# Kernel tuning notes

Measured on AMD Instinct MI355X. Metric: run time of the kernel, lower is better.

The kernel has to match this reference:

```python
import jax, jax.numpy as jnp
import numpy as np

EMB, GCN = 256, 256
N_REL = 200
B, E, TOPK = 256, 100000, 64
N_PREV, N_ENT, N_TIME = 50000, 20000, 2000


def _linear(x, w, b):
    # torch nn.Linear convention: w is [out, in]
    return x @ w.T + b


def setup_inputs() -> dict:
    key = jax.random.key(0)
    ks = jax.random.split(key, 32)
    nrm = lambda k, s: (jax.random.normal(k, s, jnp.float32) * 0.05)
    # facts columns: b, n, h, r, t, ts. b built so every batch has >= TOPK facts.
    b_col = jax.random.permutation(ks[0], jnp.arange(E, dtype=jnp.int32) % B)
    n_col = jax.random.randint(ks[1], (E,), 0, N_PREV, jnp.int32)
    h_col = jax.random.randint(ks[2], (E,), 0, N_ENT, jnp.int32)
    r_col = jax.random.randint(ks[3], (E,), 0, N_REL, jnp.int32)  # r+1 indexes [zero;rel]
    t_col = jax.random.randint(ks[4], (E,), 0, N_ENT, jnp.int32)
    ts_col = jax.random.randint(ks[5], (E,), 0, N_TIME, jnp.int32)
    facts = jnp.stack([b_col, n_col, h_col, r_col, t_col, ts_col], axis=1)
    return {
        "query_time": jax.random.randint(ks[6], (B,), 0, N_TIME, jnp.int32),  # unused by forward
        "query_emd": nrm(ks[7], (B, EMB)),
        "temp_neighbors_facts": facts,
        "ent_emd": nrm(ks[8], (N_ENT, GCN)),
        "rel_emd": nrm(ks[9], (N_REL, GCN)),
        "hidden_node": nrm(ks[10], (N_PREV, EMB)),
        "hidden_rel": nrm(ks[11], (N_PREV, EMB)),
        "hidden_time": nrm(ks[12], (N_PREV, EMB)),  # unused by forward
        "att_agg": jax.random.uniform(ks[13], (N_PREV,), jnp.float32),
        "time_emd": nrm(ks[14], (N_TIME, EMB)),
        "zero_rel_emd": nrm(ks[15], (1, GCN)),
        "W_message_w": nrm(ks[16], (EMB, 2 * EMB)), "W_message_b": jnp.zeros((EMB,), jnp.float32),
        "att_1_w": nrm(ks[17], (1, 3 * EMB)), "att_1_b": jnp.zeros((1,), jnp.float32),
        "att_2_w": nrm(ks[18], (1, EMB)), "att_2_b": jnp.zeros((1,), jnp.float32),
        "W_h_w": nrm(ks[19], (EMB, 2 * EMB)), "W_h_b": jnp.zeros((EMB,), jnp.float32),
        "lin_e_ts_w": nrm(ks[20], (EMB, GCN + EMB)), "lin_e_ts_b": jnp.zeros((EMB,), jnp.float32),
        "lin_r_ts_w": nrm(ks[21], (EMB, GCN)), "lin_r_ts_b": jnp.zeros((EMB,), jnp.float32),
        "lin_time_w": nrm(ks[22], (EMB, EMB)), "lin_time_b": jnp.zeros((EMB,), jnp.float32),
        "gru_w_ih": nrm(ks[23], (3 * EMB, EMB)), "gru_w_hh": nrm(ks[24], (3 * EMB, EMB)),
        "gru_b_ih": jnp.zeros((3 * EMB,), jnp.float32), "gru_b_hh": jnp.zeros((3 * EMB,), jnp.float32),
        "batch_size": B, "device": 0, "max_nodes": TOPK,
    }


def reference(query_time, query_emd, temp_neighbors_facts, ent_emd, rel_emd,
              hidden_node, hidden_rel, hidden_time, att_agg, time_emd,
              zero_rel_emd, W_message_w, W_message_b, att_1_w, att_1_b,
              att_2_w, att_2_b, W_h_w, W_h_b, lin_e_ts_w, lin_e_ts_b,
              lin_r_ts_w, lin_r_ts_b, lin_time_w, lin_time_b,
              gru_w_ih, gru_w_hh, gru_b_ih, gru_b_hh,
              batch_size, device, max_nodes):
    f = temp_neighbors_facts
    b, n, r, t, ts = f[:, 0], f[:, 1], f[:, 3], f[:, 4], f[:, 5]

    hidden_node_pre = hidden_node[n]            # [E, EMB]
    hidden_rel_pre = hidden_rel[n]              # [E, EMB]
    rel_all = jnp.concatenate([zero_rel_emd, rel_emd], axis=0)
    h_r = rel_all[r + 1]                        # [E, GCN]
    h_ts_raw = time_emd[ts]                     # [E, EMB]
    h_t = _linear(jnp.concatenate([ent_emd[t], h_ts_raw], -1), lin_e_ts_w, lin_e_ts_b)
    h_r = _linear(h_r, lin_r_ts_w, lin_r_ts_b)
    _ = _linear(h_ts_raw, lin_time_w, lin_time_b)  # computed but unused in original

    message = _linear(jnp.concatenate([hidden_node_pre, h_r], -1), W_message_w, W_message_b)
    att_input = jnp.concatenate([query_emd[b], message, h_t], -1)  # [E, 3*EMB]
    att1 = jax.nn.sigmoid(_linear(att_input, att_1_w, att_1_b))[:, 0]

    # single-step GRU (torch nn.GRU gate math)
    gi = h_r @ gru_w_ih.T + gru_b_ih            # [E, 3*EMB]
    gh = hidden_rel_pre @ gru_w_hh.T + gru_b_hh
    i_r, i_z, i_n = jnp.split(gi, 3, axis=-1)
    h_rg, h_zg, h_ng = jnp.split(gh, 3, axis=-1)
    rg = jax.nn.sigmoid(i_r + h_rg)
    zg = jax.nn.sigmoid(i_z + h_zg)
    ng = jnp.tanh(i_n + rg * h_ng)
    hidden_rel_new = (1.0 - zg) * ng + zg * hidden_rel_pre

    att2 = jax.nn.sigmoid(_linear(hidden_rel_new, att_2_w, att_2_b))[:, 0]
    attention = (att1 + att2) * 0.5

    # vectorized per-batch top-k (each batch is guaranteed >= max_nodes facts)
    order = jnp.lexsort((-attention, b))        # sort by batch asc, attention desc
    counts = jax.ops.segment_sum(jnp.ones_like(b), b, num_segments=batch_size)
    starts = jnp.cumsum(counts) - counts
    sel = (starts[:, None] + jnp.arange(max_nodes)[None, :]).reshape(-1)
    new_index = order[sel]                      # [B*topk]

    facts_k = f[new_index]
    message = message[new_index]
    hidden_rel_new = hidden_rel_new[new_index]
    attention = (att1[new_index] + att2[new_index]) * 0.5
    b_k, n_k = facts_k[:, 0], facts_k[:, 1]
    attention = attention * att_agg[n_k]
    M = b_k.shape[0]

    rows = facts_k[:, jnp.array([0, 4, 5])]     # (b, t, ts)
    tail_nodes, tail_index = jnp.unique(rows, axis=0, size=M, fill_value=0, return_inverse=True)
    tail_index = tail_index.reshape(-1)

    tail_emd = _linear(jnp.concatenate([ent_emd[tail_nodes[:, 1]], time_emd[tail_nodes[:, 2]]], -1),
                       lin_e_ts_w, lin_e_ts_b)

    # group_max_norm: normalize attention by per-batch sum (0/0 -> 0)
    den = jax.ops.segment_sum(attention, b_k, num_segments=batch_size)[b_k]
    safe_den = jnp.where(den != 0, den, 1.0)
    attention = jnp.where(den != 0, attention / safe_den, 0.0)

    message_agg = jax.ops.segment_sum(attention[:, None] * message, tail_index, num_segments=M)
    hidden_node_new = _linear(jnp.concatenate([message_agg, tail_emd], -1), W_h_w, W_h_b)  # act = identity
    hidden_rel_out = jax.ops.segment_sum(attention[:, None] * hidden_rel_new, tail_index, num_segments=M)
    att_agg_new = jax.ops.segment_sum(attention, tail_index, num_segments=M)
    return tail_nodes, hidden_node_new, hidden_rel_out, att_agg_new
```

## Files before the change

kernel.cpp:

```cpp
#include <hip/hip_runtime.h>
#include <hip/hip_bf16.h>

#define E_N    100000
#define B_N    256
#define TOPK   64
#define NPREV  50000
#define NENT   20000
#define NTIME  2000
#define NREL   200
#define M_OUT  16384
#define NTILE  3125

static __device__ __forceinline__ float sigm(float x){ return 1.f/(1.f+expf(-x)); }

__global__ void zero_kernel(unsigned* __restrict__ p, int n){
  int i = blockIdx.x*256 + threadIdx.x;
  if (i < n) p[i] = 0u;
}

__global__ void pack_w_kernel(const float* __restrict__ w_msg,
                              const float* __restrict__ w_hh,
                              float4* __restrict__ wP){
  int i = blockIdx.x*256 + threadIdx.x;
  if (i < 65536){
    int t = i & 255;
    int mat = (i >> 8) & 3;
    int kblk = i >> 10;
    float4 v;
    if (mat == 0) v = *(const float4*)&w_msg[(size_t)t*512 + kblk*4];
    else          v = *(const float4*)&w_hh[(size_t)((mat-1)*256 + t)*256 + kblk*4];
    wP[i] = v;
  }
}

__global__ void matvec_fused(const float* __restrict__ w_msg,
                             const float* __restrict__ lets_w,
                             const float* __restrict__ lets_b,
                             const float* __restrict__ att1w,
                             const float* __restrict__ att1b,
                             float* __restrict__ wm1a, float* __restrict__ ve,
                             float* __restrict__ vts, float* __restrict__ consts){
  int blk = blockIdx.x, t = threadIdx.x;
  if (blk == 3){
    if (t < 64){
      float p = 0.f;
      for (int d = t; d < 256; d += 64) p += lets_b[d]*att1w[512+d];
      for (int o = 32; o > 0; o >>= 1) p += __shfl_down(p, o);
      if (t == 0) consts[0] = att1b[0] + p;
    }
    return;
  }
  const float* M; int moff; const float* v; float* out;
  if (blk == 0){ M = w_msg;  moff = 0;   v = att1w+256; out = wm1a; }
  else if (blk == 1){ M = lets_w; moff = 0;   v = att1w+512; out = ve; }
  else { M = lets_w; moff = 256; v = att1w+512; out = vts; }
  float acc = 0.f;
  for (int d = 0; d < 256; ++d) acc += M[(size_t)d*512 + moff + t] * v[d];
  out[t] = acc;
}

__global__ void rows_dot_multi(
    const float* __restrict__ A0, const float* __restrict__ v0, float* __restrict__ o0, int n0,
    const float* __restrict__ A1, const float* __restrict__ v1, float* __restrict__ o1_, int n1,
    const float* __restrict__ A2, const float* __restrict__ v2, float* __restrict__ o2, int n2,
    const float* __restrict__ A3, const float* __restrict__ v3, float* __restrict__ o3, int n3,
    const float* __restrict__ A4, const float* __restrict__ v4, float* __restrict__ o4, int n4){
  int gid = blockIdx.x*256 + threadIdx.x;
  int wid = gid >> 6, lane = gid & 63;
  const float* A; const float* v; float* o; int r;
  if (wid < n0){ A=A0; v=v0; o=o0; r=wid; }
  else if ((wid -= n0) < n1){ A=A1; v=v1; o=o1_; r=wid; }
  else if ((wid -= n1) < n2){ A=A2; v=v2; o=o2; r=wid; }
  else if ((wid -= n2) < n3){ A=A3; v=v3; o=o3; r=wid; }
  else if ((wid -= n3) < n4){ A=A4; v=v4; o=o4; r=wid; }
  else return;
  const float* row = A + (size_t)r*256;
  float p = 0.f;
  for (int k = lane; k < 256; k += 64) p += row[k]*v[k];
  for (int off = 32; off > 0; off >>= 1) p += __shfl_down(p, off);
  if (lane == 0) o[r] = p;
}

template<int ND>
__global__ __launch_bounds__(256) void tile_linear(
    const float* __restrict__ A, int lda,
    const float* __restrict__ Bw, int ldb, int boff,
    const float* __restrict__ bias,
    float* __restrict__ out, int ldo, int rows){
  __shared__ float a_s[16][260];
  int tile0 = blockIdx.x*16;
  for (int idx = threadIdx.x; idx < 16*256; idx += 256){
    int i = idx >> 8, k = idx & 255;
    int row = tile0 + i;
    a_s[i][k] = (row < rows) ? A[(size_t)row*lda + k] : 0.f;
  }
  __syncthreads();
  int d = threadIdx.x;
  const float* brow[ND];
  #pragma unroll
  for (int q = 0; q < ND; ++q) brow[q] = Bw + (size_t)(d + 256*q)*ldb + boff;
  float acc[ND][16];
  #pragma unroll
  for (int q = 0; q < ND; ++q){
    float bv = bias ? bias[d + 256*q] : 0.f;
    #pragma unroll
    for (int i = 0; i < 16; ++i) acc[q][i] = bv;
  }
  for (int k = 0; k < 256; k += 4){
    float4 w[ND];
    #pragma unroll
    for (int q = 0; q < ND; ++q) w[q] = *(const float4*)(brow[q] + k);
    #pragma unroll
    for (int i = 0; i < 16; ++i){
      float4 a = *(const float4*)&a_s[i][k];
      #pragma unroll
      for (int q = 0; q < ND; ++q)
        acc[q][i] += w[q].x*a.x + w[q].y*a.y + w[q].z*a.z + w[q].w*a.w;
    }
  }
  #pragma unroll
  for (int i = 0; i < 16; ++i){
    int row = tile0 + i;
    if (row < rows){
      #pragma unroll
      for (int q = 0; q < ND; ++q) out[(size_t)row*ldo + d + 256*q] = acc[q][i];
    }
  }
}

__global__ void hist_kernel(const int* __restrict__ facts, int* __restrict__ cnt){
  int e = blockIdx.x*256 + threadIdx.x;
  if (e < E_N) atomicAdd(&cnt[facts[e*6+1] >> 4], 1);
}

__global__ void bin_scan_kernel(const int* __restrict__ cnt, int* __restrict__ off,
                                int* __restrict__ cur){
  int lane = threadIdx.x;
  int run = 0;
  for (int base = 0; base < 3136; base += 64){
    int idx = base + lane;
    int orig = (idx < NTILE) ? cnt[idx] : 0;
    int v = orig;
    for (int o = 1; o < 64; o <<= 1){ int t = __shfl_up(v, o); if (lane >= o) v += t; }
    if (idx < NTILE){ int ex = run + v - orig; off[idx] = ex; cur[idx] = ex; }
    run += __shfl(v, 63);
  }
  if (lane == 0) off[NTILE] = E_N;
}

__global__ void scatter_kernel(const int* __restrict__ facts, int* __restrict__ cur,
                               int* __restrict__ edges){
  int e = blockIdx.x*256 + threadIdx.x;
  if (e < E_N){
    int p = atomicAdd(&cur[facts[e*6+1] >> 4], 1);
    edges[p] = e;
  }
}

__global__ __launch_bounds__(256) void att_kernel(
    const float* __restrict__ hidden_rel,
    const float4* __restrict__ wP,
    const float* __restrict__ b_hh,
    const float* __restrict__ gi,
    const float* __restrict__ att2w, const float* __restrict__ att2b,
    const int* __restrict__ facts,
    const int* __restrict__ bin_off, const int* __restrict__ bin_edges,
    const float* __restrict__ qdot, const float* __restrict__ sn_m,
    const float* __restrict__ sr_m, const float* __restrict__ se,
    const float* __restrict__ st,   const float* __restrict__ consts,
    float* __restrict__ attention){
  __shared__ float gh_s[16][776];
  int tile0 = blockIdx.x*16;
  int t = threadIdx.x;

  float acc[3][16];
  #pragma unroll
  for (int q = 0; q < 3; ++q)
    #pragma unroll
    for (int p = 0; p < 16; ++p) acc[q][p] = 0.f;

  float4 w1 = wP[256 + t], w2 = wP[512 + t], w3 = wP[768 + t];
  for (int kb = 0; kb < 64; ++kb){
    int kbn = (kb + 1) & 63;
    int nb = (kbn*4)*256 + t;
    float4 nw1 = wP[nb + 256], nw2 = wP[nb + 512], nw3 = wP[nb + 768];
    int k = kb*4;
    #pragma unroll
    for (int p = 0; p < 16; ++p){
      float4 a = *(const float4*)&hidden_rel[(size_t)(tile0+p)*256 + k];
      acc[0][p] += w1.x*a.x + w1.y*a.y + w1.z*a.z + w1.w*a.w;
      acc[1][p] += w2.x*a.x + w2.y*a.y + w2.z*a.z + w2.w*a.w;
      acc[2][p] += w3.x*a.x + w3.y*a.y + w3.z*a.z + w3.w*a.w;
    }
    w1 = nw1; w2 = nw2; w3 = nw3;
  }
  #pragma unroll
  for (int q = 0; q < 3; ++q){
    float bv = b_hh[t + 256*q];
    #pragma unroll
    for (int p = 0; p < 16; ++p)
      gh_s[p][t + 256*q] = acc[q][p] + bv;
  }
  __syncthreads();

  int wv = t >> 6, l = t & 63;
  int o0 = bin_off[blockIdx.x], o1 = bin_off[blockIdx.x + 1];
  int d0 = 4*l;
  float4 a2 = *(const float4*)&att2w[d0];
  float c1 = consts[0];
  float a2b = att2b[0];
  for (int idx = o0 + wv; idx < o1; idx += 4){
    int e  = bin_edges[idx];
    int b  = facts[e*6+0], n = facts[e*6+1], r = facts[e*6+3];
    int t_ = facts[e*6+4], ts_ = facts[e*6+5];
    int nl = n - tile0;
    float4 ghr = *(const float4*)&gh_s[nl][d0];
    float4 ghz = *(const float4*)&gh_s[nl][256+d0];
    float4 ghn = *(const float4*)&gh_s[nl][512+d0];
    const float* girow = gi + (size_t)r*768;
    float4 gir = *(const float4*)&girow[d0];
    float4 giz = *(const float4*)&girow[256+d0];
    float4 gin = *(const float4*)&girow[512+d0];
    float4 hp  = *(const float4*)&hidden_rel[(size_t)n*256 + d0];
    float partial;
    {
      float rg = sigm(gir.x + ghr.x), zg = sigm(giz.x + ghz.x);
      float ng = tanhf(gin.x + rg*ghn.x);
      partial = a2.x * ((1.f - zg)*ng + zg*hp.x);
    }{
      float rg = sigm(gir.y + ghr.y), zg = sigm(giz.y + ghz.y);
      float ng = tanhf(gin.y + rg*ghn.y);
      partial += a2.y * ((1.f - zg)*ng + zg*hp.y);
    }{
      float rg = sigm(gir.z + ghr.z), zg = sigm(giz.z + ghz.z);
      float ng = tanhf(gin.z + rg*ghn.z);
      partial += a2.z * ((1.f - zg)*ng + zg*hp.z);
    }{
      float rg = sigm(gir.w + ghr.w), zg = sigm(giz.w + ghz.w);
      float ng = tanhf(gin.w + rg*ghn.w);
      partial += a2.w * ((1.f - zg)*ng + zg*hp.w);
    }
    #pragma unroll
    for (int o = 32; o > 0; o >>= 1) partial += __shfl_xor(partial, o);
    if (l == 0){
      float att2 = sigm(partial + a2b);
      float x1 = qdot[b] + sn_m[n] + sr_m[r] + se[t_] + st[ts_] + c1;
      attention[e] = 0.5f*(sigm(x1) + att2);
    }
  }
}

__global__ __launch_bounds__(256) void topk_kernel(
    const int* __restrict__ facts, const float* __restrict__ attention,
    const float* __restrict__ att_agg,
    int* __restrict__ sel_edge, float* __restrict__ att_norm,
    unsigned* __restrict__ skey, int* __restrict__ Ub){
  __shared__ float sa[512];
  __shared__ int   si[512];
  __shared__ unsigned sk[64];
  __shared__ int cnt;
  int b = blockIdx.x, tid = threadIdx.x;
  sa[tid] = -1.f; sa[tid+256] = -1.f;
  si[tid] = 0x7fffffff; si[tid+256] = 0x7fffffff;
  if (tid == 0) cnt = 0;
  __syncthreads();
  for (int e = tid; e < E_N; e += 256){
    if (facts[e*6] == b){
      int p = atomicAdd(&cnt, 1);
      if (p < 512){ sa[p] = attention[e]; si[p] = e; }
    }
  }
  __syncthreads();
  for (int k = 2; k <= 512; k <<= 1){
    for (int j = k >> 1; j > 0; j >>= 1){
      for (int i0 = tid; i0 < 512; i0 += 256){
        int l = i0 ^ j;
        if (l > i0){
          float ai = sa[i0], al = sa[l];
          int   ii = si[i0], il = si[l];
          bool lFirst = (al > ai) || (al == ai && il < ii);
          bool up = ((i0 & k) == 0);
          if (up ? lFirst : !lFirst){
            sa[i0] = al; sa[l] = ai; si[i0] = il; si[l] = ii;
          }
        }
      }
      __syncthreads();
    }
  }
  if (tid < 64){
    int e = si[tid];
    bool valid = (e != 0x7fffffff);
    if (!valid) e = 0;
    int n = facts[e*6+1];
    float a = valid ? sa[tid]*att_agg[n] : 0.f;
    float den = a;
    for (int o = 32; o > 0; o >>= 1) den += __shfl_down(den, o);
    den = __shfl(den, 0);
    float norm = (den != 0.f) ? a/den : 0.f;
    sel_edge[b*64 + tid] = e;
    att_norm[b*64 + tid] = norm;
    int t_ = facts[e*6+4], ts_ = facts[e*6+5];
    unsigned key = (((unsigned)t_) << 11) | (unsigned)ts_;
    sk[tid] = (key << 6) | (unsigned)tid;
  }
  __syncthreads();
  for (int k = 2; k <= 64; k <<= 1){
    for (int j = k >> 1; j > 0; j >>= 1){
      unsigned nv = 0; bool act = tid < 64;
      if (act){
        unsigned mine = sk[tid], other = sk[tid ^ j];
        bool up = ((tid & k) == 0);
        bool keepmin = (up == ((tid & j) == 0));
        nv = keepmin ? (mine < other ? mine : other) : (mine > other ? mine : other);
      }
      __syncthreads();
      if (act) sk[tid] = nv;
      __syncthreads();
    }
  }
  if (tid < 64){
    unsigned kk = sk[tid];
    skey[b*64 + tid] = kk;
    bool head = (tid == 0) || ((kk >> 6) != (sk[tid-1] >> 6));
    unsigned long long bal = __ballot(head);
    if (tid == 0) Ub[b] = __popcll(bal);
  }
}

__global__ void offs_scan_kernel(const int* __restrict__ Ub, int* __restrict__ offs){
  int lane = threadIdx.x;
  int run = 0;
  for (int base = 0; base < 256; base += 64){
    int orig = Ub[base + lane];
    int v = orig;
    for (int o = 1; o < 64; o <<= 1){ int t = __shfl_up(v, o); if (lane >= o) v += t; }
    offs[base + lane] = run + v - orig;
    run += __shfl(v, 63);
  }
  if (lane == 0) offs[256] = run;
}

__global__ void emit_kernel(const unsigned* __restrict__ skey, const int* __restrict__ offs,
                            int* __restrict__ us, int* __restrict__ tails,
                            float* __restrict__ out_tail){
  int b = blockIdx.x, tid = threadIdx.x;
  unsigned kk = skey[b*64 + tid];
  bool head = (tid == 0) || ((kk >> 6) != (skey[b*64 + tid - 1] >> 6));
  unsigned long long bal = __ballot(head);
  unsigned long long mask_le = (tid == 63) ? ~0ull : ((1ull << (tid+1)) - 1ull);
  int ulocal = __popcll(bal & mask_le) - 1;
  int u = offs[b] + ulocal;
  us[b*64 + tid] = u;
  if (head){
    unsigned key = kk >> 6;
    int t_ = (int)(key >> 11), ts_ = (int)(key & 2047u);
    tails[u*3+0] = b; tails[u*3+1] = t_; tails[u*3+2] = ts_;
    out_tail[u*3+0] = (float)b;
    out_tail[u*3+1] = (float)t_;
    out_tail[u*3+2] = (float)ts_;
  }
}

__global__ __launch_bounds__(256) void sel_kernel(
    const unsigned* __restrict__ skey, const int* __restrict__ sel_edge,
    const float* __restrict__ att_norm, const int* __restrict__ facts,
    const float* __restrict__ hidden_node, const float* __restrict__ hidden_rel,
    const float4* __restrict__ wP,
    const float* __restrict__ msg_r, const float* __restrict__ gi,
    const float* __restrict__ b_hh,
    float* __restrict__ msg_sel, float* __restrict__ hrn_sel){
  __shared__ int n_s[8], r_s[8];
  __shared__ float av_s[8];
  int base = blockIdx.x*8;
  int t = threadIdx.x;
  if (t < 8){
    int gs = base + t;
    int b = gs >> 6, i = gs & 63;
    int j = (int)(skey[(size_t)b*64 + i] & 63u);
    int s = b*64 + j;
    int e = sel_edge[s];
    n_s[t] = facts[e*6+1];
    r_s[t] = facts[e*6+3];
    av_s[t] = att_norm[s];
  }
  __syncthreads();

  float acc[4][8];
  #pragma unroll
  for (int q = 0; q < 4; ++q)
    #pragma unroll
    for (int e = 0; e < 8; ++e) acc[q][e] = 0.f;

  float4 w0 = wP[t], w1 = wP[256 + t], w2 = wP[512 + t], w3 = wP[768 + t];
  for (int kb = 0; kb < 64; ++kb){
    int kbn = (kb + 1) & 63;
    int nb = (kbn*4)*256 + t;
    float4 nw0 = wP[nb], nw1 = wP[nb + 256], nw2 = wP[nb + 512], nw3 = wP[nb + 768];
    int k = kb*4;
    #pragma unroll
    for (int e = 0; e < 8; ++e){
      float4 an = *(const float4*)&hidden_node[(size_t)n_s[e]*256 + k];
      float4 ah = *(const float4*)&hidden_rel[(size_t)n_s[e]*256 + k];
      acc[0][e] += w0.x*an.x + w0.y*an.y + w0.z*an.z + w0.w*an.w;
      acc[1][e] += w1.x*ah.x + w1.y*ah.y + w1.z*ah.z + w1.w*ah.w;
      acc[2][e] += w2.x*ah.x + w2.y*ah.y + w2.z*ah.z + w2.w*ah.w;
      acc[3][e] += w3.x*ah.x + w3.y*ah.y + w3.z*ah.z + w3.w*ah.w;
    }
    w0 = nw0; w1 = nw1; w2 = nw2; w3 = nw3;
  }

  float bhr = b_hh[t], bhz = b_hh[256+t], bhn = b_hh[512+t];
  #pragma unroll
  for (int e = 0; e < 8; ++e){
    int r = r_s[e]; float a = av_s[e];
    const float* girow = gi + (size_t)r*768;
    float msgv = acc[0][e] + msg_r[(size_t)r*256 + t];
    float rg = sigm(girow[t]      + acc[1][e] + bhr);
    float zg = sigm(girow[256+t]  + acc[2][e] + bhz);
    float ng = tanhf(girow[512+t] + rg*(acc[3][e] + bhn));
    float hp = hidden_rel[(size_t)n_s[e]*256 + t];
    float hrn = (1.f - zg)*ng + zg*hp;
    size_t o = (size_t)(base + e)*256 + t;
    msg_sel[o] = a*msgv;
    hrn_sel[o] = a*hrn;
  }
}

__global__ __launch_bounds__(256) void segsum_kernel(
    const unsigned* __restrict__ skey, const int* __restrict__ us,
    const float* __restrict__ att_norm,
    const float* __restrict__ msg_sel, const float* __restrict__ hrn_sel,
    float* __restrict__ msg_agg, float* __restrict__ out_hrel,
    float* __restrict__ out_aagg){
  int b = blockIdx.x, d = threadIdx.x;
  float accm = 0.f, acch = 0.f, acca = 0.f;
  int ucur = -1;
  for (int i = 0; i < 64; ++i){
    int u = us[b*64 + i];
    if (u != ucur){
      if (ucur >= 0){
        msg_agg[(size_t)ucur*256 + d] = accm;
        out_hrel[(size_t)ucur*256 + d] = acch;
        if (d == 0) out_aagg[ucur] = acca;
      }
      ucur = u; accm = 0.f; acch = 0.f; acca = 0.f;
    }
    size_t o = (size_t)(b*64 + i)*256 + d;
    accm += msg_sel[o];
    acch += hrn_sel[o];
    int j = (int)(skey[b*64 + i] & 63u);
    acca += att_norm[b*64 + j];
  }
  if (ucur >= 0){
    msg_agg[(size_t)ucur*256 + d] = accm;
    out_hrel[(size_t)ucur*256 + d] = acch;
    if (d == 0) out_aagg[ucur] = acca;
  }
}

__global__ __launch_bounds__(256) void final_kernel(
    const float* __restrict__ msg_agg, const int* __restrict__ tails,
    const float* __restrict__ ent_t, const float* __restrict__ time_t,
    const float* __restrict__ w_h, const float* __restrict__ b_h,
    float* __restrict__ out_hn){
  __shared__ float x_s[16][520];
  int tile0 = blockIdx.x*16;
  for (int idx = threadIdx.x; idx < 16*512; idx += 256){
    int i = idx >> 9, k = idx & 511;
    int u = tile0 + i;
    float v;
    if (k < 256) v = msg_agg[(size_t)u*256 + k];
    else {
      int kk = k - 256;
      v = ent_t[(size_t)tails[u*3+1]*256 + kk] + time_t[(size_t)tails[u*3+2]*256 + kk];
    }
    x_s[i][k] = v;
  }
  __syncthreads();
  int d = threadIdx.x;
  const float* wrow = w_h + (size_t)d*512;
  float bv = b_h[d];
  float acc[16];
  #pragma unroll
  for (int i = 0; i < 16; ++i) acc[i] = bv;
  for (int k = 0; k < 512; k += 4){
    float4 w = *(const float4*)(wrow + k);
    #pragma unroll
    for (int i = 0; i < 16; ++i){
      float4 a = *(const float4*)&x_s[i][k];
      acc[i] += w.x*a.x + w.y*a.y + w.z*a.z + w.w*a.w;
    }
  }
  #pragma unroll
  for (int i = 0; i < 16; ++i)
    out_hn[(size_t)(tile0+i)*256 + d] = acc[i];
}

extern "C" void kernel_launch(void* const* d_in, const int* in_sizes, int n_in,
                              void* d_out, int out_size, void* d_ws, size_t ws_size,
                              hipStream_t stream){
  const float* query_emd   = (const float*)d_in[1];
  const int*   facts       = (const int*)  d_in[2];
  const float* ent_emd     = (const float*)d_in[3];
  const float* rel_emd     = (const float*)d_in[4];
  const float* hidden_node = (const float*)d_in[5];
  const float* hidden_rel  = (const float*)d_in[6];
  const float* att_agg     = (const float*)d_in[8];
  const float* time_emd    = (const float*)d_in[9];
  const float* w_msg       = (const float*)d_in[11];
  const float* b_msg       = (const float*)d_in[12];
  const float* att1w       = (const float*)d_in[13];
  const float* att1b       = (const float*)d_in[14];
  const float* att2w       = (const float*)d_in[15];
  const float* att2b       = (const float*)d_in[16];
  const float* w_h         = (const float*)d_in[17];
  const float* b_h         = (const float*)d_in[18];
  const float* lets_w      = (const float*)d_in[19];
  const float* lets_b      = (const float*)d_in[20];
  const float* lrts_w      = (const float*)d_in[21];
  const float* lrts_b      = (const float*)d_in[22];
  const float* w_ih        = (const float*)d_in[25];
  const float* w_hh        = (const float*)d_in[26];
  const float* b_ih        = (const float*)d_in[27];
  const float* b_hh        = (const float*)d_in[28];

  char* p = (char*)d_ws;
  auto alloc = [&](size_t bytes) -> void* {
    void* r = (void*)p; p += (bytes + 255) & ~(size_t)255; return r;
  };
  int* bin_cnt  = (int*)alloc(3136*4);
  int* bin_cur  = (int*)alloc(3136*4);
  int* tails    = (int*)alloc((size_t)M_OUT*3*4);
  float* msg_agg= (float*)alloc((size_t)M_OUT*256*4);
  size_t zero_words = (3136*4 + 3136*4 + (size_t)M_OUT*3*4 + (size_t)M_OUT*256*4) / 4;
  int* bin_off  = (int*)alloc(3136*4);
  int* bin_edges= (int*)alloc(E_N*4);
  float* attention = (float*)alloc(E_N*4);
  float* qdot   = (float*)alloc(256*4);
  float* sn_m   = (float*)alloc(NPREV*4);
  float* se     = (float*)alloc(NENT*4);
  float* st     = (float*)alloc(NTIME*4);
  float* sr_m   = (float*)alloc(NREL*4);
  float* wm1a   = (float*)alloc(256*4);
  float* ve     = (float*)alloc(256*4);
  float* vts    = (float*)alloc(256*4);
  float* consts = (float*)alloc(8*4);
  float* hr2    = (float*)alloc((size_t)NREL*256*4);
  float* msg_r  = (float*)alloc((size_t)NREL*256*4);
  float* gi     = (float*)alloc((size_t)NREL*768*4);
  float* time_t = (float*)alloc((size_t)NTIME*256*4);
  float* ent_t  = (float*)alloc((size_t)NENT*256*4);
  float4* wP    = (float4*)alloc((size_t)65536*16);
  int* sel_edge = (int*)alloc(M_OUT*4);
  float* att_nrm= (float*)alloc(M_OUT*4);
  unsigned* skey= (unsigned*)alloc(M_OUT*4);
  int* Ub       = (int*)alloc(256*4);
  int* offs     = (int*)alloc(257*4);
  int* us       = (int*)alloc(M_OUT*4);
  float* msg_sel= (float*)alloc((size_t)M_OUT*256*4);
  float* hrn_sel= (float*)alloc((size_t)M_OUT*256*4);
  (void)ws_size; (void)in_sizes; (void)n_in;

  float* out_f     = (float*)d_out;
  float* out_tail  = out_f;
  float* out_hn    = out_f + (size_t)M_OUT*3;
  float* out_hrel  = out_f + (size_t)M_OUT*3 + (size_t)M_OUT*256;
  float* out_aagg  = out_f + (size_t)M_OUT*3 + (size_t)2*M_OUT*256;

  zero_kernel<<<(out_size+255)/256, 256, 0, stream>>>((unsigned*)d_out, out_size);
  zero_kernel<<<((int)zero_words+255)/256, 256, 0, stream>>>((unsigned*)bin_cnt, (int)zero_words);

  pack_w_kernel<<<256, 256, 0, stream>>>(w_msg, w_hh, wP);
  matvec_fused<<<4, 256, 0, stream>>>(w_msg, lets_w, lets_b, att1w, att1b, wm1a, ve, vts, consts);

  tile_linear<1><<<(NREL+15)/16, 256, 0, stream>>>(rel_emd, 256, lrts_w, 256, 0, lrts_b, hr2, 256, NREL);
  tile_linear<1><<<(NREL+15)/16, 256, 0, stream>>>(hr2, 256, w_msg, 512, 256, b_msg, msg_r, 256, NREL);
  tile_linear<3><<<(NREL+15)/16, 256, 0, stream>>>(hr2, 256, w_ih, 256, 0, b_ih, gi, 768, NREL);
  tile_linear<1><<<(NTIME+15)/16, 256, 0, stream>>>(time_emd, 256, lets_w, 512, 256, (const float*)nullptr, time_t, 256, NTIME);
  tile_linear<1><<<(NENT+15)/16, 256, 0, stream>>>(ent_emd, 256, lets_w, 512, 0, lets_b, ent_t, 256, NENT);

  {
    int total_rows = B_N + NPREV + NENT + NTIME + NREL;
    int blocks = (total_rows*64 + 255)/256;
    rows_dot_multi<<<blocks, 256, 0, stream>>>(
        query_emd, att1w, qdot, B_N,
        hidden_node, wm1a, sn_m, NPREV,
        ent_emd, ve, se, NENT,
        time_emd, vts, st, NTIME,
        msg_r, att1w+256, sr_m, NREL);
  }

  hist_kernel<<<(E_N+255)/256, 256, 0, stream>>>(facts, bin_cnt);
  bin_scan_kernel<<<1, 64, 0, stream>>>(bin_cnt, bin_off, bin_cur);
  scatter_kernel<<<(E_N+255)/256, 256, 0, stream>>>(facts, bin_cur, bin_edges);

  att_kernel<<<NTILE, 256, 0, stream>>>(hidden_rel, wP, b_hh, gi, att2w, att2b,
      facts, bin_off, bin_edges, qdot, sn_m, sr_m, se, st, consts, attention);

  topk_kernel<<<B_N, 256, 0, stream>>>(facts, attention, att_agg, sel_edge, att_nrm, skey, Ub);
  offs_scan_kernel<<<1, 64, 0, stream>>>(Ub, offs);
  emit_kernel<<<B_N, 64, 0, stream>>>(skey, offs, us, tails, out_tail);
  sel_kernel<<<M_OUT/8, 256, 0, stream>>>(skey, sel_edge, att_nrm, facts,
      hidden_node, hidden_rel, wP, msg_r, gi, b_hh, msg_sel, hrn_sel);
  segsum_kernel<<<B_N, 256, 0, stream>>>(skey, us, att_nrm, msg_sel, hrn_sel,
      msg_agg, out_hrel, out_aagg);
  final_kernel<<<M_OUT/16, 256, 0, stream>>>(msg_agg, tails, ent_t, time_t, w_h, b_h, out_hn);
}
```

Before: 1.190 ms.

## Bucket facts per batch for topk, halve att tiles, use packed weights in GEMVs

The per-batch topk gather used to scan all 100k facts in every block. It now reads a CSR of edges per batch, built during the same histogram, scan and scatter passes as the node-tile binning. Node tiles in the attention kernel shrink from 16 to 8 rows, which doubles the block count and lowers register use. The ent/time projections and the final W_h linear now read k-blocked float4 weight layouts packed up front, and the final kernel no longer stages through shared memory. The costs are more atomics in scatter, extra packing work, and a hidden_rel GEMV whose weight traffic is amortised over fewer rows.

```diff
diff --git a/kernel.cpp b/kernel.cpp
--- a/kernel.cpp
+++ b/kernel.cpp
@@ -9,7 +9,7 @@
 #define NTIME  2000
 #define NREL   200
 #define M_OUT  16384
-#define NTILE  3125
+#define NT8    6250
 
 static __device__ __forceinline__ float sigm(float x){ return 1.f/(1.f+expf(-x)); }
 
@@ -20,16 +20,26 @@
 
 __global__ void pack_w_kernel(const float* __restrict__ w_msg,
                               const float* __restrict__ w_hh,
-                              float4* __restrict__ wP){
+                              const float* __restrict__ lets_w,
+                              const float* __restrict__ w_h,
+                              float4* __restrict__ wP,
+                              float4* __restrict__ wPL,
+                              float4* __restrict__ wPH){
   int i = blockIdx.x*256 + threadIdx.x;
   if (i < 65536){
-    int t = i & 255;
-    int mat = (i >> 8) & 3;
-    int kblk = i >> 10;
+    int t = i & 255, mat = (i >> 8) & 3, kblk = i >> 10;
     float4 v;
     if (mat == 0) v = *(const float4*)&w_msg[(size_t)t*512 + kblk*4];
     else          v = *(const float4*)&w_hh[(size_t)((mat-1)*256 + t)*256 + kblk*4];
     wP[i] = v;
+  } else if (i < 98304){
+    int j = i - 65536;
+    int t = j & 255, mat = (j >> 8) & 1, kblk = j >> 9;
+    wPL[j] = *(const float4*)&lets_w[(size_t)t*512 + mat*256 + kblk*4];
+  } else if (i < 131072){
+    int j = i - 98304;
+    int t = j & 255, kblk = j >> 8;
+    wPH[j] = *(const float4*)&w_h[(size_t)t*512 + kblk*4];
   }
 }
 
@@ -128,32 +138,68 @@
   }
 }
 
-__global__ void hist_kernel(const int* __restrict__ facts, int* __restrict__ cnt){
+__global__ __launch_bounds__(256) void gemv_ets(
+    const float* __restrict__ act, const float4* __restrict__ wPL, int matsel,
+    const float* __restrict__ bias, float* __restrict__ out){
+  int tile0 = blockIdx.x*16, t = threadIdx.x;
+  float acc[16];
+  float bv = bias ? bias[t] : 0.f;
+  #pragma unroll
+  for (int p = 0; p < 16; ++p) acc[p] = bv;
+  float4 w = wPL[matsel*256 + t];
+  for (int kb = 0; kb < 64; ++kb){
+    int kbn = (kb + 1) & 63;
+    float4 nw = wPL[(kbn*2 + matsel)*256 + t];
+    int k = kb*4;
+    #pragma unroll
+    for (int p = 0; p < 16; ++p){
+      float4 a = *(const float4*)&act[(size_t)(tile0+p)*256 + k];
+      acc[p] += w.x*a.x + w.y*a.y + w.z*a.z + w.w*a.w;
+    }
+    w = nw;
+  }
+  #pragma unroll
+  for (int p = 0; p < 16; ++p)
+    out[(size_t)(tile0+p)*256 + t] = acc[p];
+}
+
+__global__ void hist2_kernel(const int* __restrict__ facts,
+                             int* __restrict__ cnt_t, int* __restrict__ cnt_b){
   int e = blockIdx.x*256 + threadIdx.x;
-  if (e < E_N) atomicAdd(&cnt[facts[e*6+1] >> 4], 1);
-}
-
-__global__ void bin_scan_kernel(const int* __restrict__ cnt, int* __restrict__ off,
-                                int* __restrict__ cur){
+  if (e < E_N){
+    atomicAdd(&cnt_t[facts[e*6+1] >> 3], 1);
+    atomicAdd(&cnt_b[facts[e*6+0]], 1);
+  }
+}
+
+__global__ void scan2_kernel(const int* __restrict__ cnt_t, int* __restrict__ off_t, int* __restrict__ cur_t,
+                             const int* __restrict__ cnt_b, int* __restrict__ off_b, int* __restrict__ cur_b){
+  const int* cnt; int* off; int* cur; int n;
+  if (blockIdx.x == 0){ cnt = cnt_t; off = off_t; cur = cur_t; n = NT8; }
+  else { cnt = cnt_b; off = off_b; cur = cur_b; n = B_N; }
   int lane = threadIdx.x;
   int run = 0;
-  for (int base = 0; base < 3136; base += 64){
+  int npad = (n + 63) & ~63;
+  for (int base = 0; base < npad; base += 64){
     int idx = base + lane;
-    int orig = (idx < NTILE) ? cnt[idx] : 0;
+    int orig = (idx < n) ? cnt[idx] : 0;
     int v = orig;
     for (int o = 1; o < 64; o <<= 1){ int t = __shfl_up(v, o); if (lane >= o) v += t; }
-    if (idx < NTILE){ int ex = run + v - orig; off[idx] = ex; cur[idx] = ex; }
+    if (idx < n){ int ex = run + v - orig; off[idx] = ex; cur[idx] = ex; }
     run += __shfl(v, 63);
   }
-  if (lane == 0) off[NTILE] = E_N;
-}
-
-__global__ void scatter_kernel(const int* __restrict__ facts, int* __restrict__ cur,
-                               int* __restrict__ edges){
+  if (lane == 0) off[n] = E_N;
+}
+
+__global__ void scatter2_kernel(const int* __restrict__ facts,
+                                int* __restrict__ cur_t, int* __restrict__ edges_t,
+                                int* __restrict__ cur_b, int* __restrict__ edges_b){
   int e = blockIdx.x*256 + threadIdx.x;
   if (e < E_N){
-    int p = atomicAdd(&cur[facts[e*6+1] >> 4], 1);
-    edges[p] = e;
+    int pt = atomicAdd(&cur_t[facts[e*6+1] >> 3], 1);
+    edges_t[pt] = e;
+    int pb = atomicAdd(&cur_b[facts[e*6+0]], 1);
+    edges_b[pb] = e;
   }
 }
 
@@ -169,15 +215,15 @@
     const float* __restrict__ sr_m, const float* __restrict__ se,
     const float* __restrict__ st,   const float* __restrict__ consts,
     float* __restrict__ attention){
-  __shared__ float gh_s[16][776];
-  int tile0 = blockIdx.x*16;
+  __shared__ float gh_s[8][776];
+  int tile0 = blockIdx.x*8;
   int t = threadIdx.x;
 
-  float acc[3][16];
+  float acc[3][8];
   #pragma unroll
   for (int q = 0; q < 3; ++q)
     #pragma unroll
-    for (int p = 0; p < 16; ++p) acc[q][p] = 0.f;
+    for (int p = 0; p < 8; ++p) acc[q][p] = 0.f;
 
   float4 w1 = wP[256 + t], w2 = wP[512 + t], w3 = wP[768 + t];
   for (int kb = 0; kb < 64; ++kb){
@@ -186,7 +232,7 @@
     float4 nw1 = wP[nb + 256], nw2 = wP[nb + 512], nw3 = wP[nb + 768];
     int k = kb*4;
     #pragma unroll
-    for (int p = 0; p < 16; ++p){
+    for (int p = 0; p < 8; ++p){
       float4 a = *(const float4*)&hidden_rel[(size_t)(tile0+p)*256 + k];
       acc[0][p] += w1.x*a.x + w1.y*a.y + w1.z*a.z + w1.w*a.w;
       acc[1][p] += w2.x*a.x + w2.y*a.y + w2.z*a.z + w2.w*a.w;
@@ -198,7 +244,7 @@
   for (int q = 0; q < 3; ++q){
     float bv = b_hh[t + 256*q];
     #pragma unroll
-    for (int p = 0; p < 16; ++p)
+    for (int p = 0; p < 8; ++p)
       gh_s[p][t + 256*q] = acc[q][p] + bv;
   }
   __syncthreads();
@@ -253,22 +299,20 @@
 __global__ __launch_bounds__(256) void topk_kernel(
     const int* __restrict__ facts, const float* __restrict__ attention,
     const float* __restrict__ att_agg,
+    const int* __restrict__ boff, const int* __restrict__ bedges,
     int* __restrict__ sel_edge, float* __restrict__ att_norm,
     unsigned* __restrict__ skey, int* __restrict__ Ub){
   __shared__ float sa[512];
   __shared__ int   si[512];
   __shared__ unsigned sk[64];
-  __shared__ int cnt;
   int b = blockIdx.x, tid = threadIdx.x;
   sa[tid] = -1.f; sa[tid+256] = -1.f;
   si[tid] = 0x7fffffff; si[tid+256] = 0x7fffffff;
-  if (tid == 0) cnt = 0;
   __syncthreads();
-  for (int e = tid; e < E_N; e += 256){
-    if (facts[e*6] == b){
-      int p = atomicAdd(&cnt, 1);
-      if (p < 512){ sa[p] = attention[e]; si[p] = e; }
-    }
+  int o0 = boff[b], cnt = boff[b+1] - o0;
+  for (int i = tid; i < cnt; i += 256){
+    int e = bedges[o0 + i];
+    sa[i] = attention[e]; si[i] = e;
   }
   __syncthreads();
   for (int k = 2; k <= 512; k <<= 1){
@@ -462,39 +506,46 @@
 __global__ __launch_bounds__(256) void final_kernel(
     const float* __restrict__ msg_agg, const int* __restrict__ tails,
     const float* __restrict__ ent_t, const float* __restrict__ time_t,
-    const float* __restrict__ w_h, const float* __restrict__ b_h,
+    const float4* __restrict__ wPH,
+    const float* __restrict__ b_h,
     float* __restrict__ out_hn){
-  __shared__ float x_s[16][520];
-  int tile0 = blockIdx.x*16;
-  for (int idx = threadIdx.x; idx < 16*512; idx += 256){
-    int i = idx >> 9, k = idx & 511;
-    int u = tile0 + i;
-    float v;
-    if (k < 256) v = msg_agg[(size_t)u*256 + k];
-    else {
-      int kk = k - 256;
-      v = ent_t[(size_t)tails[u*3+1]*256 + kk] + time_t[(size_t)tails[u*3+2]*256 + kk];
-    }
-    x_s[i][k] = v;
-  }
-  __syncthreads();
-  int d = threadIdx.x;
-  const float* wrow = w_h + (size_t)d*512;
-  float bv = b_h[d];
+  int tile0 = blockIdx.x*16, t = threadIdx.x;
+  int tu[16], tsu[16];
+  #pragma unroll
+  for (int p = 0; p < 16; ++p){
+    tu[p]  = tails[(tile0+p)*3+1];
+    tsu[p] = tails[(tile0+p)*3+2];
+  }
   float acc[16];
-  #pragma unroll
-  for (int i = 0; i < 16; ++i) acc[i] = bv;
-  for (int k = 0; k < 512; k += 4){
-    float4 w = *(const float4*)(wrow + k);
-    #pragma unroll
-    for (int i = 0; i < 16; ++i){
-      float4 a = *(const float4*)&x_s[i][k];
-      acc[i] += w.x*a.x + w.y*a.y + w.z*a.z + w.w*a.w;
-    }
-  }
-  #pragma unroll
-  for (int i = 0; i < 16; ++i)
-    out_hn[(size_t)(tile0+i)*256 + d] = acc[i];
+  float bv = b_h[t];
+  #pragma unroll
+  for (int p = 0; p < 16; ++p) acc[p] = bv;
+  float4 w = wPH[t];
+  for (int kb = 0; kb < 128; ++kb){
+    int kbn = (kb + 1) & 127;
+    float4 nw = wPH[kbn*256 + t];
+    if (kb < 64){
+      int k = kb*4;
+      #pragma unroll
+      for (int p = 0; p < 16; ++p){
+        float4 a = *(const float4*)&msg_agg[(size_t)(tile0+p)*256 + k];
+        acc[p] += w.x*a.x + w.y*a.y + w.z*a.z + w.w*a.w;
+      }
+    } else {
+      int k = (kb-64)*4;
+      #pragma unroll
+      for (int p = 0; p < 16; ++p){
+        float4 a1 = *(const float4*)&ent_t[(size_t)tu[p]*256 + k];
+        float4 a2 = *(const float4*)&time_t[(size_t)tsu[p]*256 + k];
+        float ax = a1.x + a2.x, ay = a1.y + a2.y, az = a1.z + a2.z, aw = a1.w + a2.w;
+        acc[p] += w.x*ax + w.y*ay + w.z*az + w.w*aw;
+      }
+    }
+    w = nw;
+  }
+  #pragma unroll
+  for (int p = 0; p < 16; ++p)
+    out_hn[(size_t)(tile0+p)*256 + t] = acc[p];
 }
 
 extern "C" void kernel_launch(void* const* d_in, const int* in_sizes, int n_in,
@@ -529,13 +580,18 @@
   auto alloc = [&](size_t bytes) -> void* {
     void* r = (void*)p; p += (bytes + 255) & ~(size_t)255; return r;
   };
-  int* bin_cnt  = (int*)alloc(3136*4);
-  int* bin_cur  = (int*)alloc(3136*4);
+  char* zstart = p;
+  int* bin_cnt  = (int*)alloc(6272*4);
+  int* bin_cur  = (int*)alloc(6272*4);
+  int* bcnt     = (int*)alloc(256*4);
+  int* bcur     = (int*)alloc(256*4);
   int* tails    = (int*)alloc((size_t)M_OUT*3*4);
   float* msg_agg= (float*)alloc((size_t)M_OUT*256*4);
-  size_t zero_words = (3136*4 + 3136*4 + (size_t)M_OUT*3*4 + (size_t)M_OUT*256*4) / 4;
-  int* bin_off  = (int*)alloc(3136*4);
+  size_t zero_words = (size_t)(p - zstart)/4;
+  int* bin_off  = (int*)alloc(6272*4);
   int* bin_edges= (int*)alloc(E_N*4);
+  int* boff     = (int*)alloc(257*4);
+  int* bedges   = (int*)alloc(E_N*4);
   float* attention = (float*)alloc(E_N*4);
   float* qdot   = (float*)alloc(256*4);
   float* sn_m   = (float*)alloc(NPREV*4);
@@ -552,6 +608,8 @@
   float* time_t = (float*)alloc((size_t)NTIME*256*4);
   float* ent_t  = (float*)alloc((size_t)NENT*256*4);
   float4* wP    = (float4*)alloc((size_t)65536*16);
+  float4* wPL   = (float4*)alloc((size_t)32768*16);
+  float4* wPH   = (float4*)alloc((size_t)32768*16);
   int* sel_edge = (int*)alloc(M_OUT*4);
   float* att_nrm= (float*)alloc(M_OUT*4);
   unsigned* skey= (unsigned*)alloc(M_OUT*4);
@@ -569,16 +627,17 @@
   float* out_aagg  = out_f + (size_t)M_OUT*3 + (size_t)2*M_OUT*256;
 
   zero_kernel<<<(out_size+255)/256, 256, 0, stream>>>((unsigned*)d_out, out_size);
-  zero_kernel<<<((int)zero_words+255)/256, 256, 0, stream>>>((unsigned*)bin_cnt, (int)zero_words);
-
-  pack_w_kernel<<<256, 256, 0, stream>>>(w_msg, w_hh, wP);
+  zero_kernel<<<((int)zero_words+255)/256, 256, 0, stream>>>((unsigned*)zstart, (int)zero_words);
+
+  pack_w_kernel<<<512, 256, 0, stream>>>(w_msg, w_hh, lets_w, w_h, wP, wPL, wPH);
   matvec_fused<<<4, 256, 0, stream>>>(w_msg, lets_w, lets_b, att1w, att1b, wm1a, ve, vts, consts);
 
   tile_linear<1><<<(NREL+15)/16, 256, 0, stream>>>(rel_emd, 256, lrts_w, 256, 0, lrts_b, hr2, 256, NREL);
   tile_linear<1><<<(NREL+15)/16, 256, 0, stream>>>(hr2, 256, w_msg, 512, 256, b_msg, msg_r, 256, NREL);
   tile_linear<3><<<(NREL+15)/16, 256, 0, stream>>>(hr2, 256, w_ih, 256, 0, b_ih, gi, 768, NREL);
-  tile_linear<1><<<(NTIME+15)/16, 256, 0, stream>>>(time_emd, 256, lets_w, 512, 256, (const float*)nullptr, time_t, 256, NTIME);
-  tile_linear<1><<<(NENT+15)/16, 256, 0, stream>>>(ent_emd, 256, lets_w, 512, 0, lets_b, ent_t, 256, NENT);
+
+  gemv_ets<<<NENT/16, 256, 0, stream>>>(ent_emd, wPL, 0, lets_b, ent_t);
+  gemv_ets<<<NTIME/16, 256, 0, stream>>>(time_emd, wPL, 1, (const float*)nullptr, time_t);
 
   {
     int total_rows = B_N + NPREV + NENT + NTIME + NREL;
@@ -591,19 +650,20 @@
         msg_r, att1w+256, sr_m, NREL);
   }
 
-  hist_kernel<<<(E_N+255)/256, 256, 0, stream>>>(facts, bin_cnt);
-  bin_scan_kernel<<<1, 64, 0, stream>>>(bin_cnt, bin_off, bin_cur);
-  scatter_kernel<<<(E_N+255)/256, 256, 0, stream>>>(facts, bin_cur, bin_edges);
-
-  att_kernel<<<NTILE, 256, 0, stream>>>(hidden_rel, wP, b_hh, gi, att2w, att2b,
+  hist2_kernel<<<(E_N+255)/256, 256, 0, stream>>>(facts, bin_cnt, bcnt);
+  scan2_kernel<<<2, 64, 0, stream>>>(bin_cnt, bin_off, bin_cur, bcnt, boff, bcur);
+  scatter2_kernel<<<(E_N+255)/256, 256, 0, stream>>>(facts, bin_cur, bin_edges, bcur, bedges);
+
+  att_kernel<<<NT8, 256, 0, stream>>>(hidden_rel, wP, b_hh, gi, att2w, att2b,
       facts, bin_off, bin_edges, qdot, sn_m, sr_m, se, st, consts, attention);
 
-  topk_kernel<<<B_N, 256, 0, stream>>>(facts, attention, att_agg, sel_edge, att_nrm, skey, Ub);
+  topk_kernel<<<B_N, 256, 0, stream>>>(facts, attention, att_agg, boff, bedges,
+      sel_edge, att_nrm, skey, Ub);
   offs_scan_kernel<<<1, 64, 0, stream>>>(Ub, offs);
   emit_kernel<<<B_N, 64, 0, stream>>>(skey, offs, us, tails, out_tail);
   sel_kernel<<<M_OUT/8, 256, 0, stream>>>(skey, sel_edge, att_nrm, facts,
       hidden_node, hidden_rel, wP, msg_r, gi, b_hh, msg_sel, hrn_sel);
   segsum_kernel<<<B_N, 256, 0, stream>>>(skey, us, att_nrm, msg_sel, hrn_sel,
       msg_agg, out_hrel, out_aagg);
-  final_kernel<<<M_OUT/16, 256, 0, stream>>>(msg_agg, tails, ent_t, time_t, w_h, b_h, out_hn);
-}
+  final_kernel<<<M_OUT/16, 256, 0, stream>>>(msg_agg, tails, ent_t, time_t, wPH, b_h, out_hn);
+}
```

Result: slower. 1.264 ms (+6.3%).
